# Kernel optimization log

Hardware: AMD Instinct MI355X
Metric: run time of the kernel (lower is better)

Reference implementation:

```python
import jax, jax.numpy as jnp
import numpy as np

B, C, W, H, NH, FF, L = 4, 200, 300, 128, 8, 512, 2
PH = H // NH
MAXLEN = 200
PE_N = 512
NEG = -1e15


def _sinusoidal_pe():
    # fairseq-style sinusoidal table, get_embedding(512, hidden_size)
    half = H // 2
    freq = np.exp(np.arange(half, dtype=np.float64) * -(np.log(10000.0) / (half - 1)))
    ang = np.arange(PE_N, dtype=np.float64)[:, None] * freq[None, :]
    return jnp.asarray(np.concatenate([np.sin(ang), np.cos(ang)], axis=1), jnp.float32)

PE = _sinusoidal_pe()  # [512, H], frozen (requires_grad=False in torch)


def setup_inputs() -> dict:
    key = jax.random.key(0)
    ks = jax.random.split(key, 20)

    def lin(k, fan_in, shape):
        lim = 1.0 / np.sqrt(fan_in)
        return jax.random.uniform(k, shape, jnp.float32, -lim, lim)

    return {
        'chars': jax.random.normal(ks[0], (B, C, H), jnp.float32),
        'words': jax.random.normal(ks[1], (B, W, H), jnp.float32),
        'pos_s': jax.random.randint(ks[2], (B, C), 0, MAXLEN),
        'pos_e': jax.random.randint(ks[3], (B, C), 0, MAXLEN),
        'lex_s': jax.random.randint(ks[4], (B, W), 0, MAXLEN),
        'lex_e': jax.random.randint(ks[5], (B, W), 0, MAXLEN),
        'seq_len': jax.random.randint(ks[6], (B,), 100, C + 1),
        'lex_num': jax.random.randint(ks[7], (B,), 150, W + 1),
        # Four_Pos_Fusion 'ff': Linear(4H -> H) + ReLU
        'Wf': lin(ks[8], 4 * H, (4 * H, H)),
        'bf': jnp.zeros((H,), jnp.float32),
        # per-layer attention / FFN params, stacked on leading layer dim
        'Wq': lin(ks[9], H, (L, H, H)),  'bq': jnp.zeros((L, H), jnp.float32),
        'Wk': lin(ks[10], H, (L, H, H)), 'bk': jnp.zeros((L, H), jnp.float32),
        'Wv': lin(ks[11], H, (L, H, H)), 'bv': jnp.zeros((L, H), jnp.float32),
        'Wr': lin(ks[12], H, (L, H, H)), 'br': jnp.zeros((L, H), jnp.float32),
        'u_bias': jax.random.normal(ks[13], (L, NH, PH), jnp.float32) * 0.02,
        'v_bias': jax.random.normal(ks[14], (L, NH, PH), jnp.float32) * 0.02,
        'ln1_g': jnp.ones((L, H), jnp.float32), 'ln1_b': jnp.zeros((L, H), jnp.float32),
        'ln2_g': jnp.ones((L, H), jnp.float32), 'ln2_b': jnp.zeros((L, H), jnp.float32),
        'W1': lin(ks[15], H, (L, H, FF)),  'b1': jnp.zeros((L, FF), jnp.float32),
        'W2': lin(ks[16], FF, (L, FF, H)), 'b2': jnp.zeros((L, H), jnp.float32),
    }


def _ln(x, g, b):
    m = jnp.mean(x, -1, keepdims=True)
    v = jnp.var(x, -1, keepdims=True)
    return (x - m) / jnp.sqrt(v + 1e-5) * g + b


def reference(chars, words, pos_s, pos_e, lex_s, lex_e, seq_len, lex_num,
              Wf, bf, Wq, bq, Wk, bk, Wv, bv, Wr, br, u_bias, v_bias,
              ln1_g, ln1_b, ln2_g, ln2_b, W1, b1, W2, b2):
    # four relative-position distance tables (char span vs word span), offset by max_seq_len
    idx = lambda p, l: jnp.clip(p[:, :, None] - l[:, None, :] + MAXLEN, 0, PE_N - 1)
    # Linear(4H->H) over the concat of four gathered PE tensors, expressed as
    # a sum of 4 chunked matmuls to avoid materializing the [B,C,W,4H] concat.
    rel = (PE[idx(pos_s, lex_s)] @ Wf[0:H] + PE[idx(pos_s, lex_e)] @ Wf[H:2 * H]
           + PE[idx(pos_e, lex_s)] @ Wf[2 * H:3 * H] + PE[idx(pos_e, lex_e)] @ Wf[3 * H:4 * H] + bf)
    rel = jax.nn.relu(rel)  # [B, C, W, H]

    # char_lex_len_to_mask: valid (char i, word j) pairs
    mask = (jnp.arange(C) < seq_len[:, None])[:, :, None] & (jnp.arange(W) < lex_num[:, None])[:, None, :]
    mask = mask[:, None]  # [B, 1, C, W]

    out = chars
    for i in range(L):
        q = (out @ Wq[i] + bq[i]).reshape(B, C, NH, PH)
        k = (words @ Wk[i] + bk[i]).reshape(B, W, NH, PH)
        v = (words @ Wv[i] + bv[i]).reshape(B, W, NH, PH)
        r = (rel @ Wr[i] + br[i]).reshape(B, C, W, NH, PH)
        A_C = jnp.einsum('bcnp,bwnp->bncw', q + u_bias[i], k)
        B_D = jnp.einsum('bcnp,bcwnp->bncw', q + v_bias[i], r)
        score = jnp.where(mask, A_C + B_D, NEG)  # scale=False
        att = jax.nn.softmax(score, axis=-1)
        att = jnp.where(mask, att, 0.0)  # dropout=0 (eval)
        ctx = jnp.einsum('bncw,bwnp->bcnp', att, v).reshape(B, C, H)
        out = _ln(ctx + out, ln1_g[i], ln1_b[i])
        ff = jax.nn.relu(out @ W1[i] + b1[i]) @ W2[i] + b2[i]
        out = _ln(ff + out, ln2_g[i], ln2_b[i])
    return out
```

## Files before the change

kernel.cpp:

```cpp
#include <hip/hip_runtime.h>
#include <math.h>

#define B_ 4
#define C_ 200
#define CH_ 100
#define W_ 300
#define WP_ 304
#define H_ 128
#define NH_ 8
#define PH_ 16
#define FF_ 512
#define L_ 2
#define MAXLEN_ 200
#define PEN_ 512
#define WVS_ 136
#define NTILE_ 19

typedef __bf16 bf16x8 __attribute__((ext_vector_type(8)));
typedef float f32x4v __attribute__((ext_vector_type(4)));

#define SEG_PEW   512
#define SEG_KV    (SEG_PEW + B_ * W_)
#define SEG_WR    (SEG_KV + 256)
#define SEG_W1T   (SEG_WR + 128)
#define PREP_BLOCKS (SEG_W1T + 128)

__global__ __launch_bounds__(128) void prep_kernel(
        const float* __restrict__ Wf, const float* __restrict__ bfv,
        const float* __restrict__ words,
        const float* __restrict__ Wk, const float* __restrict__ bk,
        const float* __restrict__ Wv, const float* __restrict__ bv,
        const float* __restrict__ Wr, const float* __restrict__ W1,
        const float* __restrict__ W2,
        __bf16* __restrict__ kb, __bf16* __restrict__ PEWb, __bf16* __restrict__ vTb,
        __bf16* __restrict__ WrB, __bf16* __restrict__ W1T, __bf16* __restrict__ W2T) {
    __shared__ __align__(16) float s_row[H_];
    __shared__ float s_tile[32][33];
    int t = threadIdx.x;
    if (blockIdx.x < SEG_PEW) {
        int p = blockIdx.x;
        {
            int j = (t < 64) ? t : (t - 64);
            double f = exp(-(double)j * (log(10000.0) / 63.0));
            double a = (double)p * f;
            s_row[t] = (float)((t < 64) ? sin(a) : cos(a));
        }
        __syncthreads();
        float acc0 = 0.f, acc1 = 0.f, acc2 = 0.f, acc3 = 0.f;
        for (int j = 0; j < H_; ++j) {
            float xv = s_row[j];
            int row = j * H_ + t;
            acc0 += xv * Wf[0 * H_ * H_ + row];
            acc1 += xv * Wf[1 * H_ * H_ + row];
            acc2 += xv * Wf[2 * H_ * H_ + row];
            acc3 += xv * Wf[3 * H_ * H_ + row];
        }
        PEWb[(0 * PEN_ + p) * H_ + t] = (__bf16)(acc0 + bfv[t]);
        PEWb[(1 * PEN_ + p) * H_ + t] = (__bf16)acc1;
        PEWb[(2 * PEN_ + p) * H_ + t] = (__bf16)acc2;
        PEWb[(3 * PEN_ + p) * H_ + t] = (__bf16)acc3;
    } else if (blockIdx.x < SEG_KV) {
        int rem = blockIdx.x - SEG_PEW;
        int bb = rem / W_, w = rem % W_;
        s_row[t] = words[rem * H_ + t];
        __syncthreads();
        const float4* row4 = (const float4*)s_row;
        #pragma unroll 1
        for (int li = 0; li < L_; ++li) {
            const float* wk = Wk + li * H_ * H_;
            const float* wv = Wv + li * H_ * H_;
            float4 ak = {0,0,0,0}, av = {0,0,0,0};
            #pragma unroll 2
            for (int g = 0; g < 32; ++g) {
                float4 x = row4[g];
                int j0 = 4 * g;
                ak.x += x.x * wk[(j0 + 0) * H_ + t];
                ak.y += x.y * wk[(j0 + 1) * H_ + t];
                ak.z += x.z * wk[(j0 + 2) * H_ + t];
                ak.w += x.w * wk[(j0 + 3) * H_ + t];
                av.x += x.x * wv[(j0 + 0) * H_ + t];
                av.y += x.y * wv[(j0 + 1) * H_ + t];
                av.z += x.z * wv[(j0 + 2) * H_ + t];
                av.w += x.w * wv[(j0 + 3) * H_ + t];
            }
            kb[(size_t)(li * B_ * W_ + rem) * H_ + t] =
                (__bf16)((ak.x + ak.y) + (ak.z + ak.w) + bk[li * H_ + t]);
            size_t vrow = ((size_t)(li * B_ + bb) * H_ + t) * WP_;
            vTb[vrow + w] = (__bf16)((av.x + av.y) + (av.z + av.w) + bv[li * H_ + t]);
            if (w == 0) {
                vTb[vrow + 300] = (__bf16)0.f; vTb[vrow + 301] = (__bf16)0.f;
                vTb[vrow + 302] = (__bf16)0.f; vTb[vrow + 303] = (__bf16)0.f;
            }
        }
    } else if (blockIdx.x < SEG_WR) {
        int i = (blockIdx.x - SEG_KV) * 128 + t;
        WrB[i] = (__bf16)Wr[i];
    } else if (blockIdx.x < SEG_W1T) {
        int blk = blockIdx.x - SEG_WR;
        int l = blk >> 6;
        int rem = blk & 63;
        int jt = rem >> 4;
        int ut = rem & 15;
        int r = t >> 5, cc = t & 31;
        #pragma unroll
        for (int k = 0; k < 8; ++k) {
            int j = jt * 32 + r + 4 * k;
            s_tile[r + 4 * k][cc] = W1[(l * H_ + j) * FF_ + ut * 32 + cc];
        }
        __syncthreads();
        int jl = t & 31, ul = t >> 5;
        #pragma unroll
        for (int k = 0; k < 8; ++k) {
            int u = ut * 32 + ul + 4 * k;
            W1T[((size_t)(l * FF_ + u)) * H_ + jt * 32 + jl] = (__bf16)s_tile[jl][ul + 4 * k];
        }
    } else {
        int blk = blockIdx.x - SEG_W1T;
        int l = blk >> 6;
        int rem = blk & 63;
        int ut = rem >> 2;
        int ht = rem & 3;
        int r = t >> 5, cc = t & 31;
        #pragma unroll
        for (int k = 0; k < 8; ++k) {
            int u = ut * 32 + r + 4 * k;
            s_tile[r + 4 * k][cc] = W2[(l * FF_ + u) * H_ + ht * 32 + cc];
        }
        __syncthreads();
        int ul = t & 31, hl = t >> 5;
        #pragma unroll
        for (int k = 0; k < 8; ++k) {
            int h = ht * 32 + hl + 4 * k;
            W2T[((size_t)(l * H_ + h)) * FF_ + ut * 32 + ul] = (__bf16)s_tile[ul][hl + 4 * k];
        }
    }
}

__global__ __launch_bounds__(256, 2) void mega_kernel(
    const float* __restrict__ chars,
    const int* __restrict__ pos_s, const int* __restrict__ pos_e,
    const int* __restrict__ lex_s, const int* __restrict__ lex_e,
    const int* __restrict__ seq_len, const int* __restrict__ lex_num,
    const float* __restrict__ Wq, const float* __restrict__ bq,
    const float* __restrict__ br,
    const float* __restrict__ u_bias, const float* __restrict__ v_bias,
    const float* __restrict__ ln1_g, const float* __restrict__ ln1_b,
    const float* __restrict__ ln2_g, const float* __restrict__ ln2_b,
    const float* __restrict__ b1, const float* __restrict__ b2,
    const __bf16* __restrict__ kb, const __bf16* __restrict__ PEWb,
    const __bf16* __restrict__ vTb, const __bf16* __restrict__ WrB,
    const __bf16* __restrict__ W1T, const __bf16* __restrict__ W2T,
    float* __restrict__ out) {

    __shared__ __align__(16) float s_x[2][H_], s_qv[2][H_];
    __shared__ __align__(16) __bf16 s_wvecb[2][16][WVS_];
    __shared__ __align__(16) __bf16 s_qub[2][16][WVS_];
    __shared__ float s_bterm[2][NH_];
    __shared__ __align__(16) float s_sc[2][NH_][WP_];
    __shared__ float s_red[2][132];
    __shared__ __align__(16) float s_hid[2][FF_];
    __shared__ float s_tmp[2][256];
    __shared__ int s_ls[W_], s_le[W_];

    int blk = blockIdx.x;
    int b = blk / CH_, c0 = blk % CH_;
    int t = threadIdx.x;
    int lane = t & 63;
    int wid = t >> 6;
    int l15 = lane & 15, quad = lane >> 4;

    if (t < H_) {
        s_x[0][t] = chars[(b * C_ + c0) * H_ + t];
        s_x[1][t] = chars[(b * C_ + c0 + CH_) * H_ + t];
    }
    for (int w = t; w < W_; w += 256) {
        s_ls[w] = lex_s[b * W_ + w];
        s_le[w] = lex_e[b * W_ + w];
    }
    for (int i = t; i < 2 * 8 * WVS_; i += 256) {
        int r = i / (8 * WVS_), rem = i % (8 * WVS_);
        s_wvecb[r][8 + rem / WVS_][rem % WVS_] = (__bf16)0.f;
    }
    for (int i = t; i < 2 * 16 * WVS_; i += 256) {
        int r = i / (16 * WVS_), rem = i % (16 * WVS_);
        s_qub[r][rem / WVS_][rem % WVS_] = (__bf16)0.f;
    }
    int ps0 = pos_s[b * C_ + c0],        pev0 = pos_e[b * C_ + c0];
    int ps1 = pos_s[b * C_ + c0 + CH_],  pev1 = pos_e[b * C_ + c0 + CH_];
    int slen = seq_len[b];
    int cvalid0 = (c0 < slen), cvalid1 = (c0 + CH_ < slen);
    int wnum = lex_num[b];
    __syncthreads();

    bf16x8 Ac0[5][4], Ac1[5][4];

    #pragma unroll
    for (int li = 0; li < L_; ++li) {
        {
            int half = t >> 7, h = t & 127;
            const float* WqL = Wq + li * H_ * H_;
            const float4* x40 = (const float4*)s_x[0];
            const float4* x41 = (const float4*)s_x[1];
            float4 a0 = {0,0,0,0}, a1 = {0,0,0,0};
            #pragma unroll 2
            for (int g = half * 16; g < half * 16 + 16; ++g) {
                float4 xa = x40[g], xb = x41[g];
                int j0 = 4 * g;
                float w0 = WqL[(j0 + 0) * H_ + h], w1 = WqL[(j0 + 1) * H_ + h];
                float w2 = WqL[(j0 + 2) * H_ + h], w3 = WqL[(j0 + 3) * H_ + h];
                a0.x += xa.x * w0; a0.y += xa.y * w1; a0.z += xa.z * w2; a0.w += xa.w * w3;
                a1.x += xb.x * w0; a1.y += xb.y * w1; a1.z += xb.z * w2; a1.w += xb.w * w3;
            }
            s_tmp[0][t] = (a0.x + a0.y) + (a0.z + a0.w);
            s_tmp[1][t] = (a1.x + a1.y) + (a1.z + a1.w);
        }
        __syncthreads();
        if (t < H_) {
            #pragma unroll
            for (int r = 0; r < 2; ++r) {
                float acc = s_tmp[r][t] + s_tmp[r][t + 128] + bq[li * H_ + t];
                s_qub[r][t >> 4][t] = (__bf16)(acc + u_bias[li * H_ + t]);
                s_qv[r][t] = acc + v_bias[li * H_ + t];
            }
        }
        __syncthreads();

        if (t < H_) {
            const __bf16* WrRow = WrB + li * H_ * H_ + t * H_;
            #pragma unroll 2
            for (int n = 0; n < NH_; ++n) {
                bf16x8 w0 = *(const bf16x8*)(WrRow + n * PH_);
                bf16x8 w1 = *(const bf16x8*)(WrRow + n * PH_ + 8);
                #pragma unroll
                for (int r = 0; r < 2; ++r) {
                    const float4* qv4 = (const float4*)(s_qv[r] + n * PH_);
                    float4 q0 = qv4[0], q1 = qv4[1], q2 = qv4[2], q3 = qv4[3];
                    float4 a4;
                    a4.x = (float)w0[0] * q0.x + (float)w1[0] * q2.x;
                    a4.y = (float)w0[1] * q0.y + (float)w1[1] * q2.y;
                    a4.z = (float)w0[2] * q0.z + (float)w1[2] * q2.z;
                    a4.w = (float)w0[3] * q0.w + (float)w1[3] * q2.w;
                    a4.x += (float)w0[4] * q1.x + (float)w1[4] * q3.x;
                    a4.y += (float)w0[5] * q1.y + (float)w1[5] * q3.y;
                    a4.z += (float)w0[6] * q1.z + (float)w1[6] * q3.z;
                    a4.w += (float)w0[7] * q1.w + (float)w1[7] * q3.w;
                    s_wvecb[r][n][t] = (__bf16)((a4.x + a4.y) + (a4.z + a4.w));
                }
            }
        } else if (t < H_ + NH_) {
            int n = t - H_;
            const float4* br4 = (const float4*)(br + li * H_ + n * PH_);
            float4 b0 = br4[0], b1v = br4[1], b2v = br4[2], b3v = br4[3];
            #pragma unroll
            for (int r = 0; r < 2; ++r) {
                const float4* qv4 = (const float4*)(s_qv[r] + n * PH_);
                float4 q0 = qv4[0], q1 = qv4[1], q2 = qv4[2], q3 = qv4[3];
                float4 a4;
                a4.x = b0.x * q0.x + b2v.x * q2.x;
                a4.y = b0.y * q0.y + b2v.y * q2.y;
                a4.z = b0.z * q0.z + b2v.z * q2.z;
                a4.w = b0.w * q0.w + b2v.w * q2.w;
                a4.x += b1v.x * q1.x + b3v.x * q3.x;
                a4.y += b1v.y * q1.y + b3v.y * q3.y;
                a4.z += b1v.z * q1.z + b3v.z * q3.z;
                a4.w += b1v.w * q1.w + b3v.w * q3.w;
                s_bterm[r][n] = (a4.x + a4.y) + (a4.z + a4.w);
            }
        }
        __syncthreads();

        const __bf16* kL = kb + (size_t)(li * B_ + b) * W_ * H_;
        {
            const __bf16* wrow0 = &s_wvecb[0][l15][0];
            const __bf16* wrow1 = &s_wvecb[1][l15][0];
            const __bf16* qrow0 = &s_qub[0][l15][0];
            const __bf16* qrow1 = &s_qub[1][l15][0];
            #pragma unroll
            for (int tc = 0; tc < 5; ++tc) {
                int tile = wid + 4 * tc;
                if (tile < NTILE_) {
                    int w0t = tile * 16;
                    int w = w0t + l15; if (w > W_ - 1) w = W_ - 1;
                    const __bf16* kr = kL + (size_t)w * H_;
                    f32x4v acc0 = {0.f,0.f,0.f,0.f}, acc1 = {0.f,0.f,0.f,0.f};
                    if (li == 0) {
                        int ls = s_ls[w], le = s_le[w];
                        int i00 = min(max(ps0 - ls + MAXLEN_, 0), PEN_ - 1);
                        int i01 = min(max(ps0 - le + MAXLEN_, 0), PEN_ - 1);
                        int i02 = min(max(pev0 - ls + MAXLEN_, 0), PEN_ - 1);
                        int i03 = min(max(pev0 - le + MAXLEN_, 0), PEN_ - 1);
                        int i10 = min(max(ps1 - ls + MAXLEN_, 0), PEN_ - 1);
                        int i11 = min(max(ps1 - le + MAXLEN_, 0), PEN_ - 1);
                        int i12 = min(max(pev1 - ls + MAXLEN_, 0), PEN_ - 1);
                        int i13 = min(max(pev1 - le + MAXLEN_, 0), PEN_ - 1);
                        const __bf16* r00 = PEWb + (size_t)(0 * PEN_ + i00) * H_;
                        const __bf16* r01 = PEWb + (size_t)(1 * PEN_ + i01) * H_;
                        const __bf16* r02 = PEWb + (size_t)(2 * PEN_ + i02) * H_;
                        const __bf16* r03 = PEWb + (size_t)(3 * PEN_ + i03) * H_;
                        const __bf16* r10 = PEWb + (size_t)(0 * PEN_ + i10) * H_;
                        const __bf16* r11 = PEWb + (size_t)(1 * PEN_ + i11) * H_;
                        const __bf16* r12 = PEWb + (size_t)(2 * PEN_ + i12) * H_;
                        const __bf16* r13 = PEWb + (size_t)(3 * PEN_ + i13) * H_;
                        #pragma unroll
                        for (int s = 0; s < 4; ++s) {
                            int h0 = s * 32 + quad * 8;
                            bf16x8 K = *(const bf16x8*)(kr + h0);
                            bf16x8 A0, A1;
                            {
                                bf16x8 t0 = *(const bf16x8*)(r00 + h0);
                                bf16x8 t1 = *(const bf16x8*)(r01 + h0);
                                bf16x8 t2 = *(const bf16x8*)(r02 + h0);
                                bf16x8 t3 = *(const bf16x8*)(r03 + h0);
                                #pragma unroll
                                for (int j = 0; j < 8; ++j)
                                    A0[j] = (__bf16)fmaxf((float)t0[j] + (float)t1[j] + (float)t2[j] + (float)t3[j], 0.f);
                            }
                            {
                                bf16x8 t0 = *(const bf16x8*)(r10 + h0);
                                bf16x8 t1 = *(const bf16x8*)(r11 + h0);
                                bf16x8 t2 = *(const bf16x8*)(r12 + h0);
                                bf16x8 t3 = *(const bf16x8*)(r13 + h0);
                                #pragma unroll
                                for (int j = 0; j < 8; ++j)
                                    A1[j] = (__bf16)fmaxf((float)t0[j] + (float)t1[j] + (float)t2[j] + (float)t3[j], 0.f);
                            }
                            Ac0[tc][s] = A0;
                            Ac1[tc][s] = A1;
                            bf16x8 Bf0 = *(const bf16x8*)(wrow0 + h0);
                            acc0 = __builtin_amdgcn_mfma_f32_16x16x32_bf16(A0, Bf0, acc0, 0, 0, 0);
                            bf16x8 Bq0 = *(const bf16x8*)(qrow0 + h0);
                            acc0 = __builtin_amdgcn_mfma_f32_16x16x32_bf16(K, Bq0, acc0, 0, 0, 0);
                            bf16x8 Bf1 = *(const bf16x8*)(wrow1 + h0);
                            acc1 = __builtin_amdgcn_mfma_f32_16x16x32_bf16(A1, Bf1, acc1, 0, 0, 0);
                            bf16x8 Bq1 = *(const bf16x8*)(qrow1 + h0);
                            acc1 = __builtin_amdgcn_mfma_f32_16x16x32_bf16(K, Bq1, acc1, 0, 0, 0);
                        }
                    } else {
                        #pragma unroll
                        for (int s = 0; s < 4; ++s) {
                            int h0 = s * 32 + quad * 8;
                            bf16x8 K = *(const bf16x8*)(kr + h0);
                            bf16x8 A0 = Ac0[tc][s];
                            bf16x8 A1 = Ac1[tc][s];
                            bf16x8 Bf0 = *(const bf16x8*)(wrow0 + h0);
                            acc0 = __builtin_amdgcn_mfma_f32_16x16x32_bf16(A0, Bf0, acc0, 0, 0, 0);
                            bf16x8 Bq0 = *(const bf16x8*)(qrow0 + h0);
                            acc0 = __builtin_amdgcn_mfma_f32_16x16x32_bf16(K, Bq0, acc0, 0, 0, 0);
                            bf16x8 Bf1 = *(const bf16x8*)(wrow1 + h0);
                            acc1 = __builtin_amdgcn_mfma_f32_16x16x32_bf16(A1, Bf1, acc1, 0, 0, 0);
                            bf16x8 Bq1 = *(const bf16x8*)(qrow1 + h0);
                            acc1 = __builtin_amdgcn_mfma_f32_16x16x32_bf16(K, Bq1, acc1, 0, 0, 0);
                        }
                    }
                    if (l15 < NH_) {
                        float bt0 = s_bterm[0][l15], bt1 = s_bterm[1][l15];
                        #pragma unroll
                        for (int r = 0; r < 4; ++r) {
                            int wr = w0t + quad * 4 + r;
                            if (wr < W_) {
                                s_sc[0][l15][wr] = acc0[r] + bt0;
                                s_sc[1][l15][wr] = acc1[r] + bt1;
                            }
                        }
                    }
                }
            }
        }
        __syncthreads();

        {
            int n = t >> 5, ln_ = t & 31;
            #pragma unroll
            for (int r = 0; r < 2; ++r) {
                int cval = r ? cvalid1 : cvalid0;
                if (cval) {
                    float m = -INFINITY;
                    for (int w = ln_; w < wnum; w += 32) m = fmaxf(m, s_sc[r][n][w]);
                    #pragma unroll
                    for (int off = 16; off > 0; off >>= 1) m = fmaxf(m, __shfl_xor(m, off, 32));
                    float sum = 0.f;
                    for (int w = ln_; w < wnum; w += 32) sum += expf(s_sc[r][n][w] - m);
                    #pragma unroll
                    for (int off = 16; off > 0; off >>= 1) sum += __shfl_xor(sum, off, 32);
                    float inv = 1.f / sum;
                    for (int w = ln_; w < WP_; w += 32)
                        s_sc[r][n][w] = (w < wnum) ? expf(s_sc[r][n][w] - m) * inv : 0.f;
                } else {
                    for (int w = ln_; w < WP_; w += 32) s_sc[r][n][w] = 0.f;
                }
            }
        }
        __syncthreads();

        {
            int h = t & 127, half = t >> 7, n = h >> 4;
            const __bf16* vrow = vTb + ((size_t)(li * B_ + b) * H_ + h) * WP_;
            const float4* att0 = (const float4*)(s_sc[0][n]);
            const float4* att1 = (const float4*)(s_sc[1][n]);
            float4 a0 = {0,0,0,0}, a1 = {0,0,0,0};
            #pragma unroll 2
            for (int g = half * 19; g < half * 19 + 19; ++g) {
                bf16x8 vv = *(const bf16x8*)(vrow + 8 * g);
                float4 p00 = att0[2 * g], p01 = att0[2 * g + 1];
                float4 p10 = att1[2 * g], p11 = att1[2 * g + 1];
                float v0 = (float)vv[0], v1 = (float)vv[1], v2 = (float)vv[2], v3 = (float)vv[3];
                float v4 = (float)vv[4], v5 = (float)vv[5], v6 = (float)vv[6], v7 = (float)vv[7];
                a0.x += p00.x * v0 + p01.x * v4;
                a0.y += p00.y * v1 + p01.y * v5;
                a0.z += p00.z * v2 + p01.z * v6;
                a0.w += p00.w * v3 + p01.w * v7;
                a1.x += p10.x * v0 + p11.x * v4;
                a1.y += p10.y * v1 + p11.y * v5;
                a1.z += p10.z * v2 + p11.z * v6;
                a1.w += p10.w * v3 + p11.w * v7;
            }
            s_tmp[0][t] = (a0.x + a0.y) + (a0.z + a0.w);
            s_tmp[1][t] = (a1.x + a1.y) + (a1.z + a1.w);
        }
        __syncthreads();

        if (t < 128) {
            s_red[0][t] = s_tmp[0][t] + s_tmp[0][t + 128] + s_x[0][t];
        } else {
            int e = t - 128;
            s_red[1][e] = s_tmp[1][e] + s_tmp[1][e + 128] + s_x[1][e];
        }
        __syncthreads();
        if (t < 128) {
            int r = t >> 6, l = t & 63;
            float a = s_red[r][l], bb = s_red[r][l + 64];
            float s = a + bb, ss = a * a + bb * bb;
            #pragma unroll
            for (int off = 32; off > 0; off >>= 1) {
                s += __shfl_down(s, off);
                ss += __shfl_down(ss, off);
            }
            if (l == 0) {
                float mean = s * (1.f / 128.f);
                float var = ss * (1.f / 128.f) - mean * mean;
                s_red[r][128] = mean;
                s_red[r][129] = rsqrtf(var + 1e-5f);
            }
        }
        __syncthreads();
        if (t < H_) {
            float g1 = ln1_g[li * H_ + t], b1v = ln1_b[li * H_ + t];
            #pragma unroll
            for (int r = 0; r < 2; ++r)
                s_x[r][t] = (s_red[r][t] - s_red[r][128]) * s_red[r][129] * g1 + b1v;
        }
        __syncthreads();

        {
            const __bf16* W1l = W1T + (size_t)li * FF_ * H_;
            int u0 = t * 2;
            const __bf16* ra = W1l + (size_t)u0 * H_;
            const __bf16* rb = W1l + (size_t)(u0 + 1) * H_;
            const float4* x40 = (const float4*)s_x[0];
            const float4* x41 = (const float4*)s_x[1];
            float4 a00 = {0,0,0,0}, a01 = {0,0,0,0}, a10 = {0,0,0,0}, a11 = {0,0,0,0};
            #pragma unroll 2
            for (int g = 0; g < 16; ++g) {
                bf16x8 wa = *(const bf16x8*)(ra + 8 * g);
                bf16x8 wb = *(const bf16x8*)(rb + 8 * g);
                float4 xa0 = x40[2 * g], xa1 = x40[2 * g + 1];
                float4 xb0 = x41[2 * g], xb1 = x41[2 * g + 1];
                a00.x += xa0.x * (float)wa[0] + xa1.x * (float)wa[4];
                a00.y += xa0.y * (float)wa[1] + xa1.y * (float)wa[5];
                a00.z += xa0.z * (float)wa[2] + xa1.z * (float)wa[6];
                a00.w += xa0.w * (float)wa[3] + xa1.w * (float)wa[7];
                a01.x += xa0.x * (float)wb[0] + xa1.x * (float)wb[4];
                a01.y += xa0.y * (float)wb[1] + xa1.y * (float)wb[5];
                a01.z += xa0.z * (float)wb[2] + xa1.z * (float)wb[6];
                a01.w += xa0.w * (float)wb[3] + xa1.w * (float)wb[7];
                a10.x += xb0.x * (float)wa[0] + xb1.x * (float)wa[4];
                a10.y += xb0.y * (float)wa[1] + xb1.y * (float)wa[5];
                a10.z += xb0.z * (float)wa[2] + xb1.z * (float)wa[6];
                a10.w += xb0.w * (float)wa[3] + xb1.w * (float)wa[7];
                a11.x += xb0.x * (float)wb[0] + xb1.x * (float)wb[4];
                a11.y += xb0.y * (float)wb[1] + xb1.y * (float)wb[5];
                a11.z += xb0.z * (float)wb[2] + xb1.z * (float)wb[6];
                a11.w += xb0.w * (float)wb[3] + xb1.w * (float)wb[7];
            }
            float bb0 = b1[li * FF_ + u0], bb1 = b1[li * FF_ + u0 + 1];
            s_hid[0][u0]     = fmaxf((a00.x + a00.y) + (a00.z + a00.w) + bb0, 0.f);
            s_hid[0][u0 + 1] = fmaxf((a01.x + a01.y) + (a01.z + a01.w) + bb1, 0.f);
            s_hid[1][u0]     = fmaxf((a10.x + a10.y) + (a10.z + a10.w) + bb0, 0.f);
            s_hid[1][u0 + 1] = fmaxf((a11.x + a11.y) + (a11.z + a11.w) + bb1, 0.f);
        }
        __syncthreads();

        {
            int half = t >> 7, h = t & 127;
            const __bf16* wrow2 = W2T + ((size_t)li * H_ + h) * FF_ + half * 256;
            const float4* h40 = (const float4*)(s_hid[0] + half * 256);
            const float4* h41 = (const float4*)(s_hid[1] + half * 256);
            float4 a0 = {0,0,0,0}, a1 = {0,0,0,0};
            #pragma unroll 2
            for (int g = 0; g < 32; ++g) {
                bf16x8 wv = *(const bf16x8*)(wrow2 + 8 * g);
                float4 p00 = h40[2 * g], p01 = h40[2 * g + 1];
                float4 p10 = h41[2 * g], p11 = h41[2 * g + 1];
                float v0 = (float)wv[0], v1 = (float)wv[1], v2 = (float)wv[2], v3 = (float)wv[3];
                float v4 = (float)wv[4], v5 = (float)wv[5], v6 = (float)wv[6], v7 = (float)wv[7];
                a0.x += p00.x * v0 + p01.x * v4;
                a0.y += p00.y * v1 + p01.y * v5;
                a0.z += p00.z * v2 + p01.z * v6;
                a0.w += p00.w * v3 + p01.w * v7;
                a1.x += p10.x * v0 + p11.x * v4;
                a1.y += p10.y * v1 + p11.y * v5;
                a1.z += p10.z * v2 + p11.z * v6;
                a1.w += p10.w * v3 + p11.w * v7;
            }
            s_tmp[0][t] = (a0.x + a0.y) + (a0.z + a0.w);
            s_tmp[1][t] = (a1.x + a1.y) + (a1.z + a1.w);
        }
        __syncthreads();

        if (t < 128) {
            s_red[0][t] = s_tmp[0][t] + s_tmp[0][t + 128] + b2[li * H_ + t] + s_x[0][t];
        } else {
            int e = t - 128;
            s_red[1][e] = s_tmp[1][e] + s_tmp[1][e + 128] + b2[li * H_ + e] + s_x[1][e];
        }
        __syncthreads();
        if (t < 128) {
            int r = t >> 6, l = t & 63;
            float a = s_red[r][l], bb = s_red[r][l + 64];
            float s = a + bb, ss = a * a + bb * bb;
            #pragma unroll
            for (int off = 32; off > 0; off >>= 1) {
                s += __shfl_down(s, off);
                ss += __shfl_down(ss, off);
            }
            if (l == 0) {
                float mean = s * (1.f / 128.f);
                float var = ss * (1.f / 128.f) - mean * mean;
                s_red[r][128] = mean;
                s_red[r][129] = rsqrtf(var + 1e-5f);
            }
        }
        __syncthreads();
        if (t < H_) {
            float g2 = ln2_g[li * H_ + t], b2v = ln2_b[li * H_ + t];
            #pragma unroll
            for (int r = 0; r < 2; ++r)
                s_x[r][t] = (s_red[r][t] - s_red[r][128]) * s_red[r][129] * g2 + b2v;
        }
        __syncthreads();
    }

    if (t < H_) {
        out[(b * C_ + c0) * H_ + t] = s_x[0][t];
        out[(b * C_ + c0 + CH_) * H_ + t] = s_x[1][t];
    }
}

extern "C" void kernel_launch(void* const* d_in, const int* in_sizes, int n_in,
                              void* d_out, int out_size, void* d_ws, size_t ws_size,
                              hipStream_t stream) {
    const float* chars  = (const float*)d_in[0];
    const float* words  = (const float*)d_in[1];
    const int* pos_s   = (const int*)d_in[2];
    const int* pos_e   = (const int*)d_in[3];
    const int* lex_s   = (const int*)d_in[4];
    const int* lex_e   = (const int*)d_in[5];
    const int* seq_len = (const int*)d_in[6];
    const int* lex_num = (const int*)d_in[7];
    const float* Wf  = (const float*)d_in[8];
    const float* bfv = (const float*)d_in[9];
    const float* Wq  = (const float*)d_in[10];
    const float* bq  = (const float*)d_in[11];
    const float* Wk  = (const float*)d_in[12];
    const float* bk  = (const float*)d_in[13];
    const float* Wv  = (const float*)d_in[14];
    const float* bv  = (const float*)d_in[15];
    const float* Wr  = (const float*)d_in[16];
    const float* br  = (const float*)d_in[17];
    const float* u_bias = (const float*)d_in[18];
    const float* v_bias = (const float*)d_in[19];
    const float* ln1_g  = (const float*)d_in[20];
    const float* ln1_b  = (const float*)d_in[21];
    const float* ln2_g  = (const float*)d_in[22];
    const float* ln2_b  = (const float*)d_in[23];
    const float* W1  = (const float*)d_in[24];
    const float* b1  = (const float*)d_in[25];
    const float* W2  = (const float*)d_in[26];
    const float* b2  = (const float*)d_in[27];

    __bf16* kb   = (__bf16*)d_ws;
    __bf16* PEWb = kb + (size_t)L_ * B_ * W_ * H_;
    __bf16* vTb  = PEWb + 4 * PEN_ * H_;
    __bf16* WrB  = vTb + (size_t)L_ * B_ * H_ * WP_;
    __bf16* W1T  = WrB + L_ * H_ * H_;
    __bf16* W2T  = W1T + L_ * H_ * FF_;

    prep_kernel<<<dim3(PREP_BLOCKS), dim3(128), 0, stream>>>(
        Wf, bfv, words, Wk, bk, Wv, bv, Wr, W1, W2,
        kb, PEWb, vTb, WrB, W1T, W2T);

    mega_kernel<<<dim3(B_ * CH_), dim3(256), 0, stream>>>(
        chars, pos_s, pos_e, lex_s, lex_e, seq_len, lex_num,
        Wq, bq, br, u_bias, v_bias,
        ln1_g, ln1_b, ln2_g, ln2_b, b1, b2,
        kb, PEWb, vTb, WrB, W1T, W2T, (float*)d_out);
}
```

Baseline: 241.1 us.

## Process one char per block and recompute relative-position tiles per layer

Changes the mega kernel from two chars per block (400 blocks) to one char per block (800 blocks), halving shared memory and register state per block and raising launch bounds to 3 blocks per SM. The cached per-layer A tiles (Ac0/Ac1 registers) are dropped, so the four PE-table gathers and the ReLU sum are recomputed in both layers. The intent is more parallelism and occupancy. The cost is that each weight read (Wq, Wr, W1, W2) is now amortized over one char instead of two, and the gather work is done twice.

```diff
diff --git a/kernel.cpp b/kernel.cpp
--- a/kernel.cpp
+++ b/kernel.cpp
@@ -136,7 +136,7 @@
     }
 }
 
-__global__ __launch_bounds__(256, 2) void mega_kernel(
+__global__ __launch_bounds__(256, 3) void mega_kernel(
     const float* __restrict__ chars,
     const int* __restrict__ pos_s, const int* __restrict__ pos_e,
     const int* __restrict__ lex_s, const int* __restrict__ lex_e,
@@ -152,76 +152,61 @@
     const __bf16* __restrict__ W1T, const __bf16* __restrict__ W2T,
     float* __restrict__ out) {
 
-    __shared__ __align__(16) float s_x[2][H_], s_qv[2][H_];
-    __shared__ __align__(16) __bf16 s_wvecb[2][16][WVS_];
-    __shared__ __align__(16) __bf16 s_qub[2][16][WVS_];
-    __shared__ float s_bterm[2][NH_];
-    __shared__ __align__(16) float s_sc[2][NH_][WP_];
-    __shared__ float s_red[2][132];
-    __shared__ __align__(16) float s_hid[2][FF_];
-    __shared__ float s_tmp[2][256];
+    __shared__ __align__(16) float s_x[H_], s_qv[H_];
+    __shared__ __align__(16) __bf16 s_wvecb[16][WVS_];
+    __shared__ __align__(16) __bf16 s_qub[16][WVS_];
+    __shared__ float s_bterm[NH_];
+    __shared__ __align__(16) float s_sc[NH_][WP_];
+    __shared__ float s_red[132];
+    __shared__ __align__(16) float s_hid[FF_];
+    __shared__ float s_tmp[256];
     __shared__ int s_ls[W_], s_le[W_];
 
     int blk = blockIdx.x;
-    int b = blk / CH_, c0 = blk % CH_;
+    int b = blk / C_, c = blk % C_;
     int t = threadIdx.x;
     int lane = t & 63;
     int wid = t >> 6;
     int l15 = lane & 15, quad = lane >> 4;
 
-    if (t < H_) {
-        s_x[0][t] = chars[(b * C_ + c0) * H_ + t];
-        s_x[1][t] = chars[(b * C_ + c0 + CH_) * H_ + t];
-    }
+    if (t < H_) s_x[t] = chars[(b * C_ + c) * H_ + t];
     for (int w = t; w < W_; w += 256) {
         s_ls[w] = lex_s[b * W_ + w];
         s_le[w] = lex_e[b * W_ + w];
     }
-    for (int i = t; i < 2 * 8 * WVS_; i += 256) {
-        int r = i / (8 * WVS_), rem = i % (8 * WVS_);
-        s_wvecb[r][8 + rem / WVS_][rem % WVS_] = (__bf16)0.f;
-    }
-    for (int i = t; i < 2 * 16 * WVS_; i += 256) {
-        int r = i / (16 * WVS_), rem = i % (16 * WVS_);
-        s_qub[r][rem / WVS_][rem % WVS_] = (__bf16)0.f;
-    }
-    int ps0 = pos_s[b * C_ + c0],        pev0 = pos_e[b * C_ + c0];
-    int ps1 = pos_s[b * C_ + c0 + CH_],  pev1 = pos_e[b * C_ + c0 + CH_];
+    for (int i = t; i < 8 * WVS_; i += 256)
+        s_wvecb[8 + i / WVS_][i % WVS_] = (__bf16)0.f;
+    for (int i = t; i < 16 * WVS_; i += 256)
+        s_qub[i / WVS_][i % WVS_] = (__bf16)0.f;
+    int ps = pos_s[b * C_ + c], pev = pos_e[b * C_ + c];
     int slen = seq_len[b];
-    int cvalid0 = (c0 < slen), cvalid1 = (c0 + CH_ < slen);
+    int cvalid = (c < slen);
     int wnum = lex_num[b];
     __syncthreads();
 
-    bf16x8 Ac0[5][4], Ac1[5][4];
-
-    #pragma unroll
+    #pragma unroll 1
     for (int li = 0; li < L_; ++li) {
         {
             int half = t >> 7, h = t & 127;
             const float* WqL = Wq + li * H_ * H_;
-            const float4* x40 = (const float4*)s_x[0];
-            const float4* x41 = (const float4*)s_x[1];
-            float4 a0 = {0,0,0,0}, a1 = {0,0,0,0};
+            const float4* x4 = (const float4*)s_x;
+            float4 a0 = {0,0,0,0};
             #pragma unroll 2
             for (int g = half * 16; g < half * 16 + 16; ++g) {
-                float4 xa = x40[g], xb = x41[g];
+                float4 xa = x4[g];
                 int j0 = 4 * g;
-                float w0 = WqL[(j0 + 0) * H_ + h], w1 = WqL[(j0 + 1) * H_ + h];
-                float w2 = WqL[(j0 + 2) * H_ + h], w3 = WqL[(j0 + 3) * H_ + h];
-                a0.x += xa.x * w0; a0.y += xa.y * w1; a0.z += xa.z * w2; a0.w += xa.w * w3;
-                a1.x += xb.x * w0; a1.y += xb.y * w1; a1.z += xb.z * w2; a1.w += xb.w * w3;
-            }
-            s_tmp[0][t] = (a0.x + a0.y) + (a0.z + a0.w);
-            s_tmp[1][t] = (a1.x + a1.y) + (a1.z + a1.w);
+                a0.x += xa.x * WqL[(j0 + 0) * H_ + h];
+                a0.y += xa.y * WqL[(j0 + 1) * H_ + h];
+                a0.z += xa.z * WqL[(j0 + 2) * H_ + h];
+                a0.w += xa.w * WqL[(j0 + 3) * H_ + h];
+            }
+            s_tmp[t] = (a0.x + a0.y) + (a0.z + a0.w);
         }
         __syncthreads();
         if (t < H_) {
-            #pragma unroll
-            for (int r = 0; r < 2; ++r) {
-                float acc = s_tmp[r][t] + s_tmp[r][t + 128] + bq[li * H_ + t];
-                s_qub[r][t >> 4][t] = (__bf16)(acc + u_bias[li * H_ + t]);
-                s_qv[r][t] = acc + v_bias[li * H_ + t];
-            }
+            float acc = s_tmp[t] + s_tmp[t + 128] + bq[li * H_ + t];
+            s_qub[t >> 4][t] = (__bf16)(acc + u_bias[li * H_ + t]);
+            s_qv[t] = acc + v_bias[li * H_ + t];
         }
         __syncthreads();
 
@@ -231,50 +216,42 @@
             for (int n = 0; n < NH_; ++n) {
                 bf16x8 w0 = *(const bf16x8*)(WrRow + n * PH_);
                 bf16x8 w1 = *(const bf16x8*)(WrRow + n * PH_ + 8);
-                #pragma unroll
-                for (int r = 0; r < 2; ++r) {
-                    const float4* qv4 = (const float4*)(s_qv[r] + n * PH_);
-                    float4 q0 = qv4[0], q1 = qv4[1], q2 = qv4[2], q3 = qv4[3];
-                    float4 a4;
-                    a4.x = (float)w0[0] * q0.x + (float)w1[0] * q2.x;
-                    a4.y = (float)w0[1] * q0.y + (float)w1[1] * q2.y;
-                    a4.z = (float)w0[2] * q0.z + (float)w1[2] * q2.z;
-                    a4.w = (float)w0[3] * q0.w + (float)w1[3] * q2.w;
-                    a4.x += (float)w0[4] * q1.x + (float)w1[4] * q3.x;
-                    a4.y += (float)w0[5] * q1.y + (float)w1[5] * q3.y;
-                    a4.z += (float)w0[6] * q1.z + (float)w1[6] * q3.z;
-                    a4.w += (float)w0[7] * q1.w + (float)w1[7] * q3.w;
-                    s_wvecb[r][n][t] = (__bf16)((a4.x + a4.y) + (a4.z + a4.w));
-                }
+                const float4* qv4 = (const float4*)(s_qv + n * PH_);
+                float4 q0 = qv4[0], q1 = qv4[1], q2 = qv4[2], q3 = qv4[3];
+                float4 a4;
+                a4.x = (float)w0[0] * q0.x + (float)w1[0] * q2.x;
+                a4.y = (float)w0[1] * q0.y + (float)w1[1] * q2.y;
+                a4.z = (float)w0[2] * q0.z + (float)w1[2] * q2.z;
+                a4.w = (float)w0[3] * q0.w + (float)w1[3] * q2.w;
+                a4.x += (float)w0[4] * q1.x + (float)w1[4] * q3.x;
+                a4.y += (float)w0[5] * q1.y + (float)w1[5] * q3.y;
+                a4.z += (float)w0[6] * q1.z + (float)w1[6] * q3.z;
+                a4.w += (float)w0[7] * q1.w + (float)w1[7] * q3.w;
+                s_wvecb[n][t] = (__bf16)((a4.x + a4.y) + (a4.z + a4.w));
             }
         } else if (t < H_ + NH_) {
             int n = t - H_;
             const float4* br4 = (const float4*)(br + li * H_ + n * PH_);
             float4 b0 = br4[0], b1v = br4[1], b2v = br4[2], b3v = br4[3];
-            #pragma unroll
-            for (int r = 0; r < 2; ++r) {
-                const float4* qv4 = (const float4*)(s_qv[r] + n * PH_);
-                float4 q0 = qv4[0], q1 = qv4[1], q2 = qv4[2], q3 = qv4[3];
-                float4 a4;
-                a4.x = b0.x * q0.x + b2v.x * q2.x;
-                a4.y = b0.y * q0.y + b2v.y * q2.y;
-                a4.z = b0.z * q0.z + b2v.z * q2.z;
-                a4.w = b0.w * q0.w + b2v.w * q2.w;
-                a4.x += b1v.x * q1.x + b3v.x * q3.x;
-                a4.y += b1v.y * q1.y + b3v.y * q3.y;
-                a4.z += b1v.z * q1.z + b3v.z * q3.z;
-                a4.w += b1v.w * q1.w + b3v.w * q3.w;
-                s_bterm[r][n] = (a4.x + a4.y) + (a4.z + a4.w);
-            }
+            const float4* qv4 = (const float4*)(s_qv + n * PH_);
+            float4 q0 = qv4[0], q1 = qv4[1], q2 = qv4[2], q3 = qv4[3];
+            float4 a4;
+            a4.x = b0.x * q0.x + b2v.x * q2.x;
+            a4.y = b0.y * q0.y + b2v.y * q2.y;
+            a4.z = b0.z * q0.z + b2v.z * q2.z;
+            a4.w = b0.w * q0.w + b2v.w * q2.w;
+            a4.x += b1v.x * q1.x + b3v.x * q3.x;
+            a4.y += b1v.y * q1.y + b3v.y * q3.y;
+            a4.z += b1v.z * q1.z + b3v.z * q3.z;
+            a4.w += b1v.w * q1.w + b3v.w * q3.w;
+            s_bterm[n] = (a4.x + a4.y) + (a4.z + a4.w);
         }
         __syncthreads();
 
         const __bf16* kL = kb + (size_t)(li * B_ + b) * W_ * H_;
         {
-            const __bf16* wrow0 = &s_wvecb[0][l15][0];
-            const __bf16* wrow1 = &s_wvecb[1][l15][0];
-            const __bf16* qrow0 = &s_qub[0][l15][0];
-            const __bf16* qrow1 = &s_qub[1][l15][0];
+            const __bf16* wrow = &s_wvecb[l15][0];
+            const __bf16* qrow = &s_qub[l15][0];
             #pragma unroll
             for (int tc = 0; tc < 5; ++tc) {
                 int tile = wid + 4 * tc;
@@ -282,85 +259,39 @@
                     int w0t = tile * 16;
                     int w = w0t + l15; if (w > W_ - 1) w = W_ - 1;
                     const __bf16* kr = kL + (size_t)w * H_;
-                    f32x4v acc0 = {0.f,0.f,0.f,0.f}, acc1 = {0.f,0.f,0.f,0.f};
-                    if (li == 0) {
-                        int ls = s_ls[w], le = s_le[w];
-                        int i00 = min(max(ps0 - ls + MAXLEN_, 0), PEN_ - 1);
-                        int i01 = min(max(ps0 - le + MAXLEN_, 0), PEN_ - 1);
-                        int i02 = min(max(pev0 - ls + MAXLEN_, 0), PEN_ - 1);
-                        int i03 = min(max(pev0 - le + MAXLEN_, 0), PEN_ - 1);
-                        int i10 = min(max(ps1 - ls + MAXLEN_, 0), PEN_ - 1);
-                        int i11 = min(max(ps1 - le + MAXLEN_, 0), PEN_ - 1);
-                        int i12 = min(max(pev1 - ls + MAXLEN_, 0), PEN_ - 1);
-                        int i13 = min(max(pev1 - le + MAXLEN_, 0), PEN_ - 1);
-                        const __bf16* r00 = PEWb + (size_t)(0 * PEN_ + i00) * H_;
-                        const __bf16* r01 = PEWb + (size_t)(1 * PEN_ + i01) * H_;
-                        const __bf16* r02 = PEWb + (size_t)(2 * PEN_ + i02) * H_;
-                        const __bf16* r03 = PEWb + (size_t)(3 * PEN_ + i03) * H_;
-                        const __bf16* r10 = PEWb + (size_t)(0 * PEN_ + i10) * H_;
-                        const __bf16* r11 = PEWb + (size_t)(1 * PEN_ + i11) * H_;
-                        const __bf16* r12 = PEWb + (size_t)(2 * PEN_ + i12) * H_;
-                        const __bf16* r13 = PEWb + (size_t)(3 * PEN_ + i13) * H_;
+                    f32x4v acc = {0.f,0.f,0.f,0.f};
+                    int ls = s_ls[w], le = s_le[w];
+                    int i0 = min(max(ps  - ls + MAXLEN_, 0), PEN_ - 1);
+                    int i1 = min(max(ps  - le + MAXLEN_, 0), PEN_ - 1);
+                    int i2 = min(max(pev - ls + MAXLEN_, 0), PEN_ - 1);
+                    int i3 = min(max(pev - le + MAXLEN_, 0), PEN_ - 1);
+                    const __bf16* r0 = PEWb + (size_t)(0 * PEN_ + i0) * H_;
+                    const __bf16* r1 = PEWb + (size_t)(1 * PEN_ + i1) * H_;
+                    const __bf16* r2 = PEWb + (size_t)(2 * PEN_ + i2) * H_;
+                    const __bf16* r3 = PEWb + (size_t)(3 * PEN_ + i3) * H_;
+                    #pragma unroll
+                    for (int s = 0; s < 4; ++s) {
+                        int h0 = s * 32 + quad * 8;
+                        bf16x8 K = *(const bf16x8*)(kr + h0);
+                        bf16x8 t0 = *(const bf16x8*)(r0 + h0);
+                        bf16x8 t1 = *(const bf16x8*)(r1 + h0);
+                        bf16x8 t2 = *(const bf16x8*)(r2 + h0);
+                        bf16x8 t3 = *(const bf16x8*)(r3 + h0);
+                        bf16x8 A;
                         #pragma unroll
-                        for (int s = 0; s < 4; ++s) {
-                            int h0 = s * 32 + quad * 8;
-                            bf16x8 K = *(const bf16x8*)(kr + h0);
-                            bf16x8 A0, A1;
-                            {
-                                bf16x8 t0 = *(const bf16x8*)(r00 + h0);
-                                bf16x8 t1 = *(const bf16x8*)(r01 + h0);
-                                bf16x8 t2 = *(const bf16x8*)(r02 + h0);
-                                bf16x8 t3 = *(const bf16x8*)(r03 + h0);
-                                #pragma unroll
-                                for (int j = 0; j < 8; ++j)
-                                    A0[j] = (__bf16)fmaxf((float)t0[j] + (float)t1[j] + (float)t2[j] + (float)t3[j], 0.f);
-                            }
-                            {
-                                bf16x8 t0 = *(const bf16x8*)(r10 + h0);
-                                bf16x8 t1 = *(const bf16x8*)(r11 + h0);
-                                bf16x8 t2 = *(const bf16x8*)(r12 + h0);
-                                bf16x8 t3 = *(const bf16x8*)(r13 + h0);
-                                #pragma unroll
-                                for (int j = 0; j < 8; ++j)
-                                    A1[j] = (__bf16)fmaxf((float)t0[j] + (float)t1[j] + (float)t2[j] + (float)t3[j], 0.f);
-                            }
-                            Ac0[tc][s] = A0;
-                            Ac1[tc][s] = A1;
-                            bf16x8 Bf0 = *(const bf16x8*)(wrow0 + h0);
-                            acc0 = __builtin_amdgcn_mfma_f32_16x16x32_bf16(A0, Bf0, acc0, 0, 0, 0);
-                            bf16x8 Bq0 = *(const bf16x8*)(qrow0 + h0);
-                            acc0 = __builtin_amdgcn_mfma_f32_16x16x32_bf16(K, Bq0, acc0, 0, 0, 0);
-                            bf16x8 Bf1 = *(const bf16x8*)(wrow1 + h0);
-                            acc1 = __builtin_amdgcn_mfma_f32_16x16x32_bf16(A1, Bf1, acc1, 0, 0, 0);
-                            bf16x8 Bq1 = *(const bf16x8*)(qrow1 + h0);
-                            acc1 = __builtin_amdgcn_mfma_f32_16x16x32_bf16(K, Bq1, acc1, 0, 0, 0);
-                        }
-                    } else {
-                        #pragma unroll
-                        for (int s = 0; s < 4; ++s) {
-                            int h0 = s * 32 + quad * 8;
-                            bf16x8 K = *(const bf16x8*)(kr + h0);
-                            bf16x8 A0 = Ac0[tc][s];
-                            bf16x8 A1 = Ac1[tc][s];
-                            bf16x8 Bf0 = *(const bf16x8*)(wrow0 + h0);
-                            acc0 = __builtin_amdgcn_mfma_f32_16x16x32_bf16(A0, Bf0, acc0, 0, 0, 0);
-                            bf16x8 Bq0 = *(const bf16x8*)(qrow0 + h0);
-                            acc0 = __builtin_amdgcn_mfma_f32_16x16x32_bf16(K, Bq0, acc0, 0, 0, 0);
-                            bf16x8 Bf1 = *(const bf16x8*)(wrow1 + h0);
-                            acc1 = __builtin_amdgcn_mfma_f32_16x16x32_bf16(A1, Bf1, acc1, 0, 0, 0);
-                            bf16x8 Bq1 = *(const bf16x8*)(qrow1 + h0);
-                            acc1 = __builtin_amdgcn_mfma_f32_16x16x32_bf16(K, Bq1, acc1, 0, 0, 0);
-                        }
+                        for (int j = 0; j < 8; ++j)
+                            A[j] = (__bf16)fmaxf((float)t0[j] + (float)t1[j] + (float)t2[j] + (float)t3[j], 0.f);
+                        bf16x8 Bf = *(const bf16x8*)(wrow + h0);
+                        acc = __builtin_amdgcn_mfma_f32_16x16x32_bf16(A, Bf, acc, 0, 0, 0);
+                        bf16x8 Bq = *(const bf16x8*)(qrow + h0);
+                        acc = __builtin_amdgcn_mfma_f32_16x16x32_bf16(K, Bq, acc, 0, 0, 0);
                     }
                     if (l15 < NH_) {
-                        float bt0 = s_bterm[0][l15], bt1 = s_bterm[1][l15];
+                        float bt = s_bterm[l15];
                         #pragma unroll
                         for (int r = 0; r < 4; ++r) {
                             int wr = w0t + quad * 4 + r;
-                            if (wr < W_) {
-                                s_sc[0][l15][wr] = acc0[r] + bt0;
-                                s_sc[1][l15][wr] = acc1[r] + bt1;
-                            }
+                            if (wr < W_) s_sc[l15][wr] = acc[r] + bt;
                         }
                     }
                 }
@@ -370,24 +301,20 @@
 
         {
             int n = t >> 5, ln_ = t & 31;
-            #pragma unroll
-            for (int r = 0; r < 2; ++r) {
-                int cval = r ? cvalid1 : cvalid0;
-                if (cval) {
-                    float m = -INFINITY;
-                    for (int w = ln_; w < wnum; w += 32) m = fmaxf(m, s_sc[r][n][w]);
-                    #pragma unroll
-                    for (int off = 16; off > 0; off >>= 1) m = fmaxf(m, __shfl_xor(m, off, 32));
-                    float sum = 0.f;
-                    for (int w = ln_; w < wnum; w += 32) sum += expf(s_sc[r][n][w] - m);
-                    #pragma unroll
-                    for (int off = 16; off > 0; off >>= 1) sum += __shfl_xor(sum, off, 32);
-                    float inv = 1.f / sum;
-                    for (int w = ln_; w < WP_; w += 32)
-                        s_sc[r][n][w] = (w < wnum) ? expf(s_sc[r][n][w] - m) * inv : 0.f;
-                } else {
-                    for (int w = ln_; w < WP_; w += 32) s_sc[r][n][w] = 0.f;
-                }
+            if (cvalid) {
+                float m = -INFINITY;
+                for (int w = ln_; w < wnum; w += 32) m = fmaxf(m, s_sc[n][w]);
+                #pragma unroll
+                for (int off = 16; off > 0; off >>= 1) m = fmaxf(m, __shfl_xor(m, off, 32));
+                float sum = 0.f;
+                for (int w = ln_; w < wnum; w += 32) sum += expf(s_sc[n][w] - m);
+                #pragma unroll
+                for (int off = 16; off > 0; off >>= 1) sum += __shfl_xor(sum, off, 32);
+                float inv = 1.f / sum;
+                for (int w = ln_; w < WP_; w += 32)
+                    s_sc[n][w] = (w < wnum) ? expf(s_sc[n][w] - m) * inv : 0.f;
+            } else {
+                for (int w = ln_; w < WP_; w += 32) s_sc[n][w] = 0.f;
             }
         }
         __syncthreads();
@@ -395,59 +322,42 @@
         {
             int h = t & 127, half = t >> 7, n = h >> 4;
             const __bf16* vrow = vTb + ((size_t)(li * B_ + b) * H_ + h) * WP_;
-            const float4* att0 = (const float4*)(s_sc[0][n]);
-            const float4* att1 = (const float4*)(s_sc[1][n]);
-            float4 a0 = {0,0,0,0}, a1 = {0,0,0,0};
+            const float4* att = (const float4*)(s_sc[n]);
+            float4 a0 = {0,0,0,0};
             #pragma unroll 2
             for (int g = half * 19; g < half * 19 + 19; ++g) {
                 bf16x8 vv = *(const bf16x8*)(vrow + 8 * g);
-                float4 p00 = att0[2 * g], p01 = att0[2 * g + 1];
-                float4 p10 = att1[2 * g], p11 = att1[2 * g + 1];
-                float v0 = (float)vv[0], v1 = (float)vv[1], v2 = (float)vv[2], v3 = (float)vv[3];
-                float v4 = (float)vv[4], v5 = (float)vv[5], v6 = (float)vv[6], v7 = (float)vv[7];
-                a0.x += p00.x * v0 + p01.x * v4;
-                a0.y += p00.y * v1 + p01.y * v5;
-                a0.z += p00.z * v2 + p01.z * v6;
-                a0.w += p00.w * v3 + p01.w * v7;
-                a1.x += p10.x * v0 + p11.x * v4;
-                a1.y += p10.y * v1 + p11.y * v5;
-                a1.z += p10.z * v2 + p11.z * v6;
-                a1.w += p10.w * v3 + p11.w * v7;
-            }
-            s_tmp[0][t] = (a0.x + a0.y) + (a0.z + a0.w);
-            s_tmp[1][t] = (a1.x + a1.y) + (a1.z + a1.w);
-        }
-        __syncthreads();
-
-        if (t < 128) {
-            s_red[0][t] = s_tmp[0][t] + s_tmp[0][t + 128] + s_x[0][t];
-        } else {
-            int e = t - 128;
-            s_red[1][e] = s_tmp[1][e] + s_tmp[1][e + 128] + s_x[1][e];
-        }
-        __syncthreads();
-        if (t < 128) {
-            int r = t >> 6, l = t & 63;
-            float a = s_red[r][l], bb = s_red[r][l + 64];
+                float4 p0 = att[2 * g], p1 = att[2 * g + 1];
+                a0.x += p0.x * (float)vv[0] + p1.x * (float)vv[4];
+                a0.y += p0.y * (float)vv[1] + p1.y * (float)vv[5];
+                a0.z += p0.z * (float)vv[2] + p1.z * (float)vv[6];
+                a0.w += p0.w * (float)vv[3] + p1.w * (float)vv[7];
+            }
+            s_tmp[t] = (a0.x + a0.y) + (a0.z + a0.w);
+        }
+        __syncthreads();
+
+        if (t < 128) s_red[t] = s_tmp[t] + s_tmp[t + 128] + s_x[t];
+        __syncthreads();
+        if (t < 64) {
+            float a = s_red[t], bb = s_red[t + 64];
             float s = a + bb, ss = a * a + bb * bb;
             #pragma unroll
             for (int off = 32; off > 0; off >>= 1) {
                 s += __shfl_down(s, off);
                 ss += __shfl_down(ss, off);
             }
-            if (l == 0) {
+            if (t == 0) {
                 float mean = s * (1.f / 128.f);
                 float var = ss * (1.f / 128.f) - mean * mean;
-                s_red[r][128] = mean;
-                s_red[r][129] = rsqrtf(var + 1e-5f);
+                s_red[128] = mean;
+                s_red[129] = rsqrtf(var + 1e-5f);
             }
         }
         __syncthreads();
         if (t < H_) {
             float g1 = ln1_g[li * H_ + t], b1v = ln1_b[li * H_ + t];
-            #pragma unroll
-            for (int r = 0; r < 2; ++r)
-                s_x[r][t] = (s_red[r][t] - s_red[r][128]) * s_red[r][129] * g1 + b1v;
+            s_x[t] = (s_red[t] - s_red[128]) * s_red[129] * g1 + b1v;
         }
         __syncthreads();
 
@@ -455,105 +365,73 @@
             const __bf16* W1l = W1T + (size_t)li * FF_ * H_;
             int u0 = t * 2;
             const __bf16* ra = W1l + (size_t)u0 * H_;
-            const __bf16* rb = W1l + (size_t)(u0 + 1) * H_;
-            const float4* x40 = (const float4*)s_x[0];
-            const float4* x41 = (const float4*)s_x[1];
-            float4 a00 = {0,0,0,0}, a01 = {0,0,0,0}, a10 = {0,0,0,0}, a11 = {0,0,0,0};
+            const __bf16* rb = ra + H_;
+            const float4* x4 = (const float4*)s_x;
+            float4 a00 = {0,0,0,0}, a01 = {0,0,0,0};
             #pragma unroll 2
             for (int g = 0; g < 16; ++g) {
                 bf16x8 wa = *(const bf16x8*)(ra + 8 * g);
                 bf16x8 wb = *(const bf16x8*)(rb + 8 * g);
-                float4 xa0 = x40[2 * g], xa1 = x40[2 * g + 1];
-                float4 xb0 = x41[2 * g], xb1 = x41[2 * g + 1];
-                a00.x += xa0.x * (float)wa[0] + xa1.x * (float)wa[4];
-                a00.y += xa0.y * (float)wa[1] + xa1.y * (float)wa[5];
-                a00.z += xa0.z * (float)wa[2] + xa1.z * (float)wa[6];
-                a00.w += xa0.w * (float)wa[3] + xa1.w * (float)wa[7];
-                a01.x += xa0.x * (float)wb[0] + xa1.x * (float)wb[4];
-                a01.y += xa0.y * (float)wb[1] + xa1.y * (float)wb[5];
-                a01.z += xa0.z * (float)wb[2] + xa1.z * (float)wb[6];
-                a01.w += xa0.w * (float)wb[3] + xa1.w * (float)wb[7];
-                a10.x += xb0.x * (float)wa[0] + xb1.x * (float)wa[4];
-                a10.y += xb0.y * (float)wa[1] + xb1.y * (float)wa[5];
-                a10.z += xb0.z * (float)wa[2] + xb1.z * (float)wa[6];
-                a10.w += xb0.w * (float)wa[3] + xb1.w * (float)wa[7];
-                a11.x += xb0.x * (float)wb[0] + xb1.x * (float)wb[4];
-                a11.y += xb0.y * (float)wb[1] + xb1.y * (float)wb[5];
-                a11.z += xb0.z * (float)wb[2] + xb1.z * (float)wb[6];
-                a11.w += xb0.w * (float)wb[3] + xb1.w * (float)wb[7];
+                float4 x0 = x4[2 * g], x1 = x4[2 * g + 1];
+                a00.x += x0.x * (float)wa[0] + x1.x * (float)wa[4];
+                a00.y += x0.y * (float)wa[1] + x1.y * (float)wa[5];
+                a00.z += x0.z * (float)wa[2] + x1.z * (float)wa[6];
+                a00.w += x0.w * (float)wa[3] + x1.w * (float)wa[7];
+                a01.x += x0.x * (float)wb[0] + x1.x * (float)wb[4];
+                a01.y += x0.y * (float)wb[1] + x1.y * (float)wb[5];
+                a01.z += x0.z * (float)wb[2] + x1.z * (float)wb[6];
+                a01.w += x0.w * (float)wb[3] + x1.w * (float)wb[7];
             }
             float bb0 = b1[li * FF_ + u0], bb1 = b1[li * FF_ + u0 + 1];
-            s_hid[0][u0]     = fmaxf((a00.x + a00.y) + (a00.z + a00.w) + bb0, 0.f);
-            s_hid[0][u0 + 1] = fmaxf((a01.x + a01.y) + (a01.z + a01.w) + bb1, 0.f);
-            s_hid[1][u0]     = fmaxf((a10.x + a10.y) + (a10.z + a10.w) + bb0, 0.f);
-            s_hid[1][u0 + 1] = fmaxf((a11.x + a11.y) + (a11.z + a11.w) + bb1, 0.f);
+            s_hid[u0]     = fmaxf((a00.x + a00.y) + (a00.z + a00.w) + bb0, 0.f);
+            s_hid[u0 + 1] = fmaxf((a01.x + a01.y) + (a01.z + a01.w) + bb1, 0.f);
         }
         __syncthreads();
 
         {
             int half = t >> 7, h = t & 127;
             const __bf16* wrow2 = W2T + ((size_t)li * H_ + h) * FF_ + half * 256;
-            const float4* h40 = (const float4*)(s_hid[0] + half * 256);
-            const float4* h41 = (const float4*)(s_hid[1] + half * 256);
-            float4 a0 = {0,0,0,0}, a1 = {0,0,0,0};
+            const float4* h4 = (const float4*)(s_hid + half * 256);
+            float4 a0 = {0,0,0,0};
             #pragma unroll 2
             for (int g = 0; g < 32; ++g) {
                 bf16x8 wv = *(const bf16x8*)(wrow2 + 8 * g);
-                float4 p00 = h40[2 * g], p01 = h40[2 * g + 1];
-                float4 p10 = h41[2 * g], p11 = h41[2 * g + 1];
-                float v0 = (float)wv[0], v1 = (float)wv[1], v2 = (float)wv[2], v3 = (float)wv[3];
-                float v4 = (float)wv[4], v5 = (float)wv[5], v6 = (float)wv[6], v7 = (float)wv[7];
-                a0.x += p00.x * v0 + p01.x * v4;
-                a0.y += p00.y * v1 + p01.y * v5;
-                a0.z += p00.z * v2 + p01.z * v6;
-                a0.w += p00.w * v3 + p01.w * v7;
-                a1.x += p10.x * v0 + p11.x * v4;
-                a1.y += p10.y * v1 + p11.y * v5;
-                a1.z += p10.z * v2 + p11.z * v6;
-                a1.w += p10.w * v3 + p11.w * v7;
-            }
-            s_tmp[0][t] = (a0.x + a0.y) + (a0.z + a0.w);
-            s_tmp[1][t] = (a1.x + a1.y) + (a1.z + a1.w);
-        }
-        __syncthreads();
-
-        if (t < 128) {
-            s_red[0][t] = s_tmp[0][t] + s_tmp[0][t + 128] + b2[li * H_ + t] + s_x[0][t];
-        } else {
-            int e = t - 128;
-            s_red[1][e] = s_tmp[1][e] + s_tmp[1][e + 128] + b2[li * H_ + e] + s_x[1][e];
-        }
-        __syncthreads();
-        if (t < 128) {
-            int r = t >> 6, l = t & 63;
-            float a = s_red[r][l], bb = s_red[r][l + 64];
+                float4 p0 = h4[2 * g], p1 = h4[2 * g + 1];
+                a0.x += p0.x * (float)wv[0] + p1.x * (float)wv[4];
+                a0.y += p0.y * (float)wv[1] + p1.y * (float)wv[5];
+                a0.z += p0.z * (float)wv[2] + p1.z * (float)wv[6];
+                a0.w += p0.w * (float)wv[3] + p1.w * (float)wv[7];
+            }
+            s_tmp[t] = (a0.x + a0.y) + (a0.z + a0.w);
+        }
+        __syncthreads();
+
+        if (t < 128) s_red[t] = s_tmp[t] + s_tmp[t + 128] + b2[li * H_ + t] + s_x[t];
+        __syncthreads();
+        if (t < 64) {
+            float a = s_red[t], bb = s_red[t + 64];
             float s = a + bb, ss = a * a + bb * bb;
             #pragma unroll
             for (int off = 32; off > 0; off >>= 1) {
                 s += __shfl_down(s, off);
                 ss += __shfl_down(ss, off);
             }
-            if (l == 0) {
+            if (t == 0) {
                 float mean = s * (1.f / 128.f);
                 float var = ss * (1.f / 128.f) - mean * mean;
-                s_red[r][128] = mean;
-                s_red[r][129] = rsqrtf(var + 1e-5f);
+                s_red[128] = mean;
+                s_red[129] = rsqrtf(var + 1e-5f);
             }
         }
         __syncthreads();
         if (t < H_) {
             float g2 = ln2_g[li * H_ + t], b2v = ln2_b[li * H_ + t];
-            #pragma unroll
-            for (int r = 0; r < 2; ++r)
-                s_x[r][t] = (s_red[r][t] - s_red[r][128]) * s_red[r][129] * g2 + b2v;
+            s_x[t] = (s_red[t] - s_red[128]) * s_red[129] * g2 + b2v;
         }
         __syncthreads();
     }
 
-    if (t < H_) {
-        out[(b * C_ + c0) * H_ + t] = s_x[0][t];
-        out[(b * C_ + c0 + CH_) * H_ + t] = s_x[1][t];
-    }
+    if (t < H_) out[(b * C_ + c) * H_ + t] = s_x[t];
 }
 
 extern "C" void kernel_launch(void* const* d_in, const int* in_sizes, int n_in,
@@ -599,7 +477,7 @@
         Wf, bfv, words, Wk, bk, Wv, bv, Wr, W1, W2,
         kb, PEWb, vTb, WrB, W1T, W2T);
 
-    mega_kernel<<<dim3(B_ * CH_), dim3(256), 0, stream>>>(
+    mega_kernel<<<dim3(B_ * C_), dim3(256), 0, stream>>>(
         chars, pos_s, pos_e, lex_s, lex_e, seq_len, lex_num,
         Wq, bq, br, u_bias, v_bias,
         ln1_g, ln1_b, ln2_g, ln2_b, b1, b2,
```

Result: slower. 319.0 us (+32.3%).
